# Performance work log

Measured on AMD Instinct MI355X. Metric: run time of the kernel, lower is better.

## Reference

```python
import jax, jax.numpy as jnp
import numpy as np

B, K, F, INCH, OUTCH, R = 16, 8, 512, 512, 512, 8


def setup_inputs() -> dict:
    key = jax.random.key(0)
    ks = jax.random.split(key, 10)
    inp = {
        "x": jax.random.normal(ks[0], (B, K, F, INCH), jnp.float32),
        "u": jax.random.normal(ks[1], (B, K, OUTCH, R), jnp.float32),
        "v": jax.random.normal(ks[2], (B, K, INCH, R), jnp.float32),
        "b": jax.random.normal(ks[3], (B, 1, 1, OUTCH), jnp.float32) * 0.02,
        # learned parameters (torch nn.Linear layout: W [out, in])
        "W_pass": jax.random.normal(ks[4], (INCH // 2, INCH), jnp.float32) * 0.02,
        "b_pass": jax.random.normal(ks[5], (INCH // 2,), jnp.float32) * 0.02,
        "W_ave": jax.random.normal(ks[6], (INCH // 2, INCH), jnp.float32) * 0.02,
        "b_ave": jax.random.normal(ks[7], (INCH // 2,), jnp.float32) * 0.02,
        "W_out": jax.random.normal(ks[8], (OUTCH, INCH), jnp.float32) * 0.02,
        "b_out": jax.random.normal(ks[9], (OUTCH,), jnp.float32) * 0.02,
    }
    return inp


def reference(x, u, v, b, W_pass, b_pass, W_ave, b_ave, W_out, b_out):
    # x: [B,K,F,inch]
    k = x.shape[1]
    # 'ave' branch: linear -> mean over K -> broadcast back to K
    y = jnp.einsum('bkfi,hi->bkfh', x, W_ave) + b_ave        # [B,K,F,inch//2]
    y = jnp.broadcast_to(jnp.mean(y, axis=1, keepdims=True), y.shape)
    # 'pass' branch
    xp = jnp.einsum('bkfi,hi->bkfh', x, W_pass) + b_pass      # [B,K,F,inch//2]
    h = jnp.concatenate([xp, y], axis=-1)                     # [B,K,F,inch]
    h = jax.nn.gelu(h, approximate=False)                     # dropout is identity in eval
    # LoRA term: mean(v * h) over inch, then mean(u * z) over R
    inch = h.shape[-1]
    r = v.shape[-1]
    z = jnp.einsum('bkfi,bkir->bkfr', h, v) / inch            # [B,K,F,R]
    lora = jnp.einsum('bkfr,bkor->bkfo', z, u) / r            # [B,K,F,outch]
    out = jnp.einsum('bkfi,oi->bkfo', h, W_out) + b_out + lora + b
    out = jax.nn.gelu(out, approximate=False)
    return out
```

## Files before the change

kernel.cpp:

```cpp
#include <hip/hip_runtime.h>
#include <stdint.h>


typedef __attribute__((ext_vector_type(8))) __bf16 bf16x8;
typedef __attribute__((ext_vector_type(4))) float f32x4;
typedef __attribute__((ext_vector_type(8))) unsigned short ushort8;
typedef __attribute__((ext_vector_type(4))) unsigned short ushort4_t;
typedef __attribute__((ext_vector_type(4))) float float4_t;

#define MFMA16(a, b, c) __builtin_amdgcn_mfma_f32_16x16x32_bf16((a), (b), (c), 0, 0, 0)
#define GLL16(g, l)                                                                   \
    __builtin_amdgcn_global_load_lds((const __attribute__((address_space(1))) void*)(g), \
                                     (__attribute__((address_space(3))) void*)(l), 16, 0, 0)

__device__ inline unsigned short f2bf(float f) {
    union { float fv; unsigned u; } un; un.fv = f;
    unsigned u = un.u;
    u += 0x7FFFu + ((u >> 16) & 1u);
    return (unsigned short)(u >> 16);
}

__device__ inline float geluf(float x) {
    float x2 = x * x;
    float inner = x + 0.044715f * x * x2;
    float e = __expf(-1.5957691216057308f * inner);
    return x * __builtin_amdgcn_rcpf(1.0f + e);
}

__device__ inline bf16x8 lds8(const unsigned short* p) {
    return __builtin_bit_cast(bf16x8, *(const ushort8*)p);
}

__device__ inline void stage_w(const unsigned short* __restrict__ src, long rowbase,
                               long stride, int k0, unsigned short* buf, int l) {
#pragma unroll
    for (int it = 0; it < 4; ++it) {
        const int s = it * 64 + l;
        const int r = s >> 2;
        const int j = (s & 3) ^ (r & 3);
        GLL16(src + (rowbase + r) * stride + k0 + j * 8, &buf[it * 512]);
    }
}

__device__ inline bf16x8 ldw(const unsigned short* buf, int rbase, int l) {
    const int r = rbase + (l & 15);
    const int j = l >> 4;
    return lds8(&buf[r * 32 + (((j ^ r) & 3) << 3)]);
}

__global__ void cvt_all(const float* __restrict__ a, const float* __restrict__ b,
                        const float* __restrict__ c, unsigned short* __restrict__ oa,
                        unsigned short* __restrict__ ob, unsigned short* __restrict__ oc) {
    int bid = blockIdx.x;
    const float* s; unsigned short* d; int off;
    if (bid < 128) { s = a; d = oa; off = bid; }
    else if (bid < 256) { s = b; d = ob; off = bid - 128; }
    else { s = c; d = oc; off = bid - 256; }
    int i = off * 256 + threadIdx.x;
    float4_t v = *(const float4_t*)(s + (size_t)i * 4);
    ushort4_t r;
    r[0] = f2bf(v[0]); r[1] = f2bf(v[1]); r[2] = f2bf(v[2]); r[3] = f2bf(v[3]);
    *(ushort4_t*)(d + (size_t)i * 4) = r;
}

__global__ void mean_cvt(const float* __restrict__ x,
                         unsigned short* __restrict__ xb,
                         unsigned short* __restrict__ xm) {
    int gid = blockIdx.x * 256 + threadIdx.x;
    int c  = gid & 63;
    int bf = gid >> 6;
    int b  = bf >> 9;
    int f  = bf & 511;
    float s0 = 0.f, s1 = 0.f, s2 = 0.f, s3 = 0.f, s4 = 0.f, s5 = 0.f, s6 = 0.f, s7 = 0.f;
#pragma unroll
    for (int k = 0; k < 8; ++k) {
        long row = (long)(b * 8 + k) * 512 + f;
        float4_t lo = *(const float4_t*)(x + row * 512 + c * 8);
        float4_t hi = *(const float4_t*)(x + row * 512 + c * 8 + 4);
        s0 += lo[0]; s1 += lo[1]; s2 += lo[2]; s3 += lo[3];
        s4 += hi[0]; s5 += hi[1]; s6 += hi[2]; s7 += hi[3];
        ushort8 t;
        t[0] = f2bf(lo[0]); t[1] = f2bf(lo[1]); t[2] = f2bf(lo[2]); t[3] = f2bf(lo[3]);
        t[4] = f2bf(hi[0]); t[5] = f2bf(hi[1]); t[6] = f2bf(hi[2]); t[7] = f2bf(hi[3]);
        *(ushort8*)(xb + row * 512 + c * 8) = t;
    }
    ushort8 m;
    m[0] = f2bf(s0 * 0.125f); m[1] = f2bf(s1 * 0.125f);
    m[2] = f2bf(s2 * 0.125f); m[3] = f2bf(s3 * 0.125f);
    m[4] = f2bf(s4 * 0.125f); m[5] = f2bf(s5 * 0.125f);
    m[6] = f2bf(s6 * 0.125f); m[7] = f2bf(s7 * 0.125f);
    *(ushort8*)(xm + (long)bf * 512 + c * 8) = m;
}

__launch_bounds__(256)
__global__ void gemm_gelu(const unsigned short* __restrict__ A,
                          const unsigned short* __restrict__ W,
                          const float* __restrict__ bias,
                          unsigned short* __restrict__ O,
                          int chunk) {
    __shared__ __align__(16) unsigned short S[32768];
    const int tid = threadIdx.x;
    const int w = tid >> 6, l = tid & 63;
    const int wr = w >> 1, wc = w & 1;
    const int work = ((blockIdx.x & 7) * chunk) + (blockIdx.x >> 3);
    const int nt = work & 1;
    const int mt = work >> 1;
    const long row0 = (long)mt * 128 + wr * 64;
    const long col0 = (long)nt * 128 + wc * 64;

    unsigned short* aw[2] = { &S[w * 4096],        &S[16384 + w * 4096] };
    unsigned short* bw[2] = { &S[w * 4096 + 2048], &S[16384 + w * 4096 + 2048] };

    f32x4 acc[4][4];
    const f32x4 z4 = {0.f, 0.f, 0.f, 0.f};
#pragma unroll
    for (int i = 0; i < 4; ++i)
#pragma unroll
        for (int j = 0; j < 4; ++j) acc[i][j] = z4;

    stage_w(A, row0, 512, 0, aw[0], l);
    stage_w(W, col0, 512, 0, bw[0], l);

#pragma unroll
    for (int t = 0; t < 16; ++t) {
        if (t < 15) {
            stage_w(A, row0, 512, (t + 1) * 32, aw[(t + 1) & 1], l);
            stage_w(W, col0, 512, (t + 1) * 32, bw[(t + 1) & 1], l);
            asm volatile("s_waitcnt vmcnt(8)" ::: "memory");
        } else {
            asm volatile("s_waitcnt vmcnt(0)" ::: "memory");
        }
        const unsigned short* ab = aw[t & 1];
        const unsigned short* bb = bw[t & 1];
        bf16x8 af[4], bfr[4];
#pragma unroll
        for (int mi = 0; mi < 4; ++mi) af[mi] = ldw(ab, mi * 16, l);
#pragma unroll
        for (int nj = 0; nj < 4; ++nj) bfr[nj] = ldw(bb, nj * 16, l);
        __builtin_amdgcn_s_setprio(1);
#pragma unroll
        for (int mi = 0; mi < 4; ++mi)
#pragma unroll
            for (int nj = 0; nj < 4; ++nj)
                acc[mi][nj] = MFMA16(af[mi], bfr[nj], acc[mi][nj]);
        __builtin_amdgcn_s_setprio(0);
    }

    __syncthreads();
#pragma unroll
    for (int mi = 0; mi < 4; ++mi) {
        const int R0 = wr * 64 + mi * 16 + (l >> 4) * 4;
#pragma unroll
        for (int nj = 0; nj < 4; ++nj) {
            const int C = wc * 64 + nj * 16 + (l & 15);
            const float bv = bias[((col0 & ~63L) - wc * 64) + C];
#pragma unroll
            for (int q = 0; q < 4; ++q)
                S[(R0 + q) * 136 + C] = f2bf(geluf(acc[mi][nj][q] + bv));
        }
    }
    __syncthreads();
    const long rowt = (long)mt * 128;
    const long colt = (long)nt * 128;
#pragma unroll
    for (int s = 0; s < 8; ++s) {
        const int flat = s * 2048 + tid * 8;
        const int row = flat >> 7;
        const int col = flat & 127;
        ushort8 vv = *(const ushort8*)&S[row * 136 + col];
        *(ushort8*)(O + (rowt + row) * 256 + colt + col) = vv;
    }
}

__launch_bounds__(256)
__global__ void zcalc_s(const unsigned short* __restrict__ Hp,
                        const unsigned short* __restrict__ Gy,
                        const float* __restrict__ v,
                        unsigned short* __restrict__ zb) {
    __shared__ __align__(16) unsigned short Vt[16 * 536];
    const int tid = threadIdx.x;
    const int w = tid >> 6, l = tid & 63;
    const int mt = blockIdx.x;
    const long row0 = (long)mt * 128;
    const int gb = (mt >> 5) * 512 + (mt & 3) * 128;
    {
        ushort8 zz = {0, 0, 0, 0, 0, 0, 0, 0};
        for (int i = tid; i < (16 * 536) / 8; i += 256) *(ushort8*)&Vt[i * 8] = zz;
        __syncthreads();
        const float* vp = v + (long)(mt >> 2) * 4096;
#pragma unroll
        for (int p = 0; p < 4; ++p) {
            float4_t vv = *(const float4_t*)(vp + tid * 16 + p * 4);
#pragma unroll
            for (int j = 0; j < 4; ++j) {
                int flat = tid * 16 + p * 4 + j;
                Vt[(flat & 7) * 536 + (flat >> 3)] = f2bf(vv[j] * (1.0f / 512.0f));
            }
        }
        __syncthreads();
    }
    const unsigned short* ph[2];
    const unsigned short* pg[2];
#pragma unroll
    for (int q = 0; q < 2; ++q) {
        const int r = (w * 2 + q) * 16 + (l & 15);
        ph[q] = Hp + (row0 + r) * 256 + (l >> 4) * 8;
        pg[q] = Gy + (size_t)(gb + r) * 256 + (l >> 4) * 8;
    }
    f32x4 zacc[2];
    const f32x4 z4 = {0.f, 0.f, 0.f, 0.f};
    zacc[0] = z4; zacc[1] = z4;
#pragma unroll
    for (int ks = 0; ks < 8; ++ks) {
        bf16x8 bv = lds8(&Vt[(l & 15) * 536 + ks * 32 + (l >> 4) * 8]);
#pragma unroll
        for (int q = 0; q < 2; ++q)
            zacc[q] = MFMA16(lds8(ph[q] + ks * 32), bv, zacc[q]);
    }
#pragma unroll
    for (int ks = 0; ks < 8; ++ks) {
        bf16x8 bv = lds8(&Vt[(l & 15) * 536 + 256 + ks * 32 + (l >> 4) * 8]);
#pragma unroll
        for (int q = 0; q < 2; ++q)
            zacc[q] = MFMA16(lds8(pg[q] + ks * 32), bv, zacc[q]);
    }
    if ((l & 15) < 8) {
#pragma unroll
        for (int q = 0; q < 2; ++q) {
            const int fr = w * 2 + q;
#pragma unroll
            for (int reg = 0; reg < 4; ++reg) {
                long r = row0 + fr * 16 + (l >> 4) * 4 + reg;
                zb[r * 8 + (l & 15)] = f2bf(zacc[q][reg]);
            }
        }
    }
}

__launch_bounds__(256)
__global__ void gemm_out(const unsigned short* __restrict__ Hp,
                         const unsigned short* __restrict__ Gy,
                         const unsigned short* __restrict__ Wo,
                         const float* __restrict__ bo,
                         const float* __restrict__ bb,
                         const float* __restrict__ u,
                         const unsigned short* __restrict__ zb,
                         float* __restrict__ Out) {
    __shared__ __align__(16) char SM[67584];
    unsigned short* S = (unsigned short*)SM;
    float* Sf = (float*)SM;
    const int tid = threadIdx.x;
    const int w = tid >> 6, l = tid & 63;
    const int wr = w >> 1, wc = w & 1;
    const int work = ((blockIdx.x & 7) * 256) + (blockIdx.x >> 3);
    const int nt = work & 3;
    const int mt = work >> 2;
    const long row0 = (long)mt * 128;
    const long arow = row0 + wr * 64;
    const long grow = (long)((mt >> 5) * 512 + (mt & 3) * 128) + wr * 64;
    const long col0 = (long)nt * 128 + wc * 64;
    const int bk = mt >> 2;
    const int bi = bk >> 3;

    unsigned short* aw[2] = { &S[w * 4096],        &S[16384 + w * 4096] };
    unsigned short* bw[2] = { &S[w * 4096 + 2048], &S[16384 + w * 4096 + 2048] };

    f32x4 acc[4][4];
    const f32x4 z4 = {0.f, 0.f, 0.f, 0.f};
#pragma unroll
    for (int i = 0; i < 4; ++i)
#pragma unroll
        for (int j = 0; j < 4; ++j) acc[i][j] = z4;

    stage_w(Hp, arow, 256, 0, aw[0], l);
    stage_w(Wo, col0, 512, 0, bw[0], l);

#pragma unroll
    for (int t = 0; t < 16; ++t) {
        if (t < 15) {
            const int tt = t + 1;
            if (tt < 8) stage_w(Hp, arow, 256, tt * 32, aw[tt & 1], l);
            else        stage_w(Gy, grow, 256, (tt - 8) * 32, aw[tt & 1], l);
            stage_w(Wo, col0, 512, tt * 32, bw[tt & 1], l);
            asm volatile("s_waitcnt vmcnt(8)" ::: "memory");
        } else {
            asm volatile("s_waitcnt vmcnt(0)" ::: "memory");
        }
        const unsigned short* ab = aw[t & 1];
        const unsigned short* bbuf = bw[t & 1];
        bf16x8 af[4], bfr[4];
#pragma unroll
        for (int mi = 0; mi < 4; ++mi) af[mi] = ldw(ab, mi * 16, l);
#pragma unroll
        for (int nj = 0; nj < 4; ++nj) bfr[nj] = ldw(bbuf, nj * 16, l);
        __builtin_amdgcn_s_setprio(1);
#pragma unroll
        for (int mi = 0; mi < 4; ++mi)
#pragma unroll
            for (int nj = 0; nj < 4; ++nj)
                acc[mi][nj] = MFMA16(af[mi], bfr[nj], acc[mi][nj]);
        __builtin_amdgcn_s_setprio(0);
    }

    __syncthreads();
    {
        ushort8 zz = {0, 0, 0, 0, 0, 0, 0, 0};
        const int row = tid >> 1;
        if ((tid & 1) == 0) {
            *(ushort8*)&S[row * 32]     = *(const ushort8*)&zb[(row0 + row) * 8];
            *(ushort8*)&S[row * 32 + 8] = zz;
        } else {
            *(ushort8*)&S[row * 32 + 16] = zz;
            *(ushort8*)&S[row * 32 + 24] = zz;
        }
    }
    __syncthreads();

    const float* up = u + (long)bk * 4096;
#pragma unroll
    for (int nj = 0; nj < 4; ++nj) {
        const long og = col0 + nj * 16 + (l & 15);
        ushort8 ubits = {0, 0, 0, 0, 0, 0, 0, 0};
        if ((l >> 4) == 0) {
            float4_t u0 = *(const float4_t*)(up + og * 8);
            float4_t u1 = *(const float4_t*)(up + og * 8 + 4);
            ubits[0] = f2bf(u0[0] * 0.125f); ubits[1] = f2bf(u0[1] * 0.125f);
            ubits[2] = f2bf(u0[2] * 0.125f); ubits[3] = f2bf(u0[3] * 0.125f);
            ubits[4] = f2bf(u1[0] * 0.125f); ubits[5] = f2bf(u1[1] * 0.125f);
            ubits[6] = f2bf(u1[2] * 0.125f); ubits[7] = f2bf(u1[3] * 0.125f);
        }
        bf16x8 ub = __builtin_bit_cast(bf16x8, ubits);
#pragma unroll
        for (int mi = 0; mi < 4; ++mi) {
            bf16x8 az = lds8(&S[(wr * 64 + mi * 16 + (l & 15)) * 32 + (l >> 4) * 8]);
            acc[mi][nj] = MFMA16(az, ub, acc[mi][nj]);
        }
    }

    __syncthreads();
#pragma unroll
    for (int nj = 0; nj < 4; ++nj) {
        const long og = col0 + nj * 16 + (l & 15);
        const float badd = bo[og] + bb[bi * 512 + og];
        const int C = wc * 64 + nj * 16 + (l & 15);
#pragma unroll
        for (int mi = 0; mi < 4; ++mi) {
            const int R0 = wr * 64 + mi * 16 + (l >> 4) * 4;
#pragma unroll
            for (int q = 0; q < 4; ++q)
                Sf[(R0 + q) * 132 + C] = geluf(acc[mi][nj][q] + badd);
        }
    }
    __syncthreads();
    const long colt = (long)nt * 128;
#pragma unroll
    for (int s = 0; s < 16; ++s) {
        const int flat = s * 1024 + tid * 4;
        const int row = flat >> 7;
        const int col = flat & 127;
        float4_t vv = *(const float4_t*)&Sf[row * 132 + col];
        __builtin_nontemporal_store(vv, (float4_t*)(Out + (row0 + row) * 512 + colt + col));
    }
}

extern "C" void kernel_launch(void* const* d_in, const int* in_sizes, int n_in,
                              void* d_out, int out_size, void* d_ws, size_t ws_size,
                              hipStream_t stream) {
    const float* x  = (const float*)d_in[0];
    const float* u  = (const float*)d_in[1];
    const float* v  = (const float*)d_in[2];
    const float* bb = (const float*)d_in[3];
    const float* Wp = (const float*)d_in[4];
    const float* bp = (const float*)d_in[5];
    const float* Wa = (const float*)d_in[6];
    const float* ba = (const float*)d_in[7];
    const float* Wo = (const float*)d_in[8];
    const float* bo = (const float*)d_in[9];
    float* out = (float*)d_out;

    char* ws = (char*)d_ws;
    unsigned short* xb  = (unsigned short*)(ws + 0);
    unsigned short* zb  = (unsigned short*)(ws + 0);
    unsigned short* xm  = (unsigned short*)(ws + 67108864);
    unsigned short* gy  = (unsigned short*)(ws + 75497472);
    unsigned short* hp  = (unsigned short*)(ws + 79691776);
    unsigned short* Wpb = (unsigned short*)(ws + 113246208);
    unsigned short* Wab = (unsigned short*)(ws + 113508352);
    unsigned short* Wob = (unsigned short*)(ws + 113770496);

    cvt_all<<<512, 256, 0, stream>>>(Wp, Wa, Wo, Wpb, Wab, Wob);
    mean_cvt<<<2048, 256, 0, stream>>>(x, xb, xm);
    gemm_gelu<<<128, 256, 0, stream>>>(xm, Wab, ba, gy, 16);
    gemm_gelu<<<1024, 256, 0, stream>>>(xb, Wpb, bp, hp, 128);
    zcalc_s<<<512, 256, 0, stream>>>(hp, gy, v, zb);
    gemm_out<<<2048, 256, 0, stream>>>(hp, gy, Wob, bo, bb, u, zb, out);
}
```

Before: 169.0 us.

## Load GEMM operands directly from global into registers with 3-stage prefetch

```diff
diff --git a/kernel.cpp b/kernel.cpp
--- a/kernel.cpp
+++ b/kernel.cpp
@@ -9,9 +9,6 @@
 typedef __attribute__((ext_vector_type(4))) float float4_t;
 
 #define MFMA16(a, b, c) __builtin_amdgcn_mfma_f32_16x16x32_bf16((a), (b), (c), 0, 0, 0)
-#define GLL16(g, l)                                                                   \
-    __builtin_amdgcn_global_load_lds((const __attribute__((address_space(1))) void*)(g), \
-                                     (__attribute__((address_space(3))) void*)(l), 16, 0, 0)
 
 __device__ inline unsigned short f2bf(float f) {
     union { float fv; unsigned u; } un; un.fv = f;
@@ -29,23 +26,6 @@
 
 __device__ inline bf16x8 lds8(const unsigned short* p) {
     return __builtin_bit_cast(bf16x8, *(const ushort8*)p);
-}
-
-__device__ inline void stage_w(const unsigned short* __restrict__ src, long rowbase,
-                               long stride, int k0, unsigned short* buf, int l) {
-#pragma unroll
-    for (int it = 0; it < 4; ++it) {
-        const int s = it * 64 + l;
-        const int r = s >> 2;
-        const int j = (s & 3) ^ (r & 3);
-        GLL16(src + (rowbase + r) * stride + k0 + j * 8, &buf[it * 512]);
-    }
-}
-
-__device__ inline bf16x8 ldw(const unsigned short* buf, int rbase, int l) {
-    const int r = rbase + (l & 15);
-    const int j = l >> 4;
-    return lds8(&buf[r * 32 + (((j ^ r) & 3) << 3)]);
 }
 
 __global__ void cvt_all(const float* __restrict__ a, const float* __restrict__ b,
@@ -92,13 +72,13 @@
     *(ushort8*)(xm + (long)bf * 512 + c * 8) = m;
 }
 
-__launch_bounds__(256)
+__launch_bounds__(256, 2)
 __global__ void gemm_gelu(const unsigned short* __restrict__ A,
                           const unsigned short* __restrict__ W,
                           const float* __restrict__ bias,
                           unsigned short* __restrict__ O,
                           int chunk) {
-    __shared__ __align__(16) unsigned short S[32768];
+    __shared__ __align__(16) unsigned short S[17408];
     const int tid = threadIdx.x;
     const int w = tid >> 6, l = tid & 63;
     const int wr = w >> 1, wc = w & 1;
@@ -108,8 +88,8 @@
     const long row0 = (long)mt * 128 + wr * 64;
     const long col0 = (long)nt * 128 + wc * 64;
 
-    unsigned short* aw[2] = { &S[w * 4096],        &S[16384 + w * 4096] };
-    unsigned short* bw[2] = { &S[w * 4096 + 2048], &S[16384 + w * 4096 + 2048] };
+    const unsigned short* abase = A + (row0 + (l & 15)) * 512 + (l >> 4) * 8;
+    const unsigned short* wbase = W + (col0 + (l & 15)) * 512 + (l >> 4) * 8;
 
     f32x4 acc[4][4];
     const f32x4 z4 = {0.f, 0.f, 0.f, 0.f};
@@ -118,42 +98,47 @@
 #pragma unroll
         for (int j = 0; j < 4; ++j) acc[i][j] = z4;
 
-    stage_w(A, row0, 512, 0, aw[0], l);
-    stage_w(W, col0, 512, 0, bw[0], l);
+    ushort8 ap[3][4], bp[3][4];
+
+#define LDAB_G(st, t)                                                          \
+    {                                                                          \
+        _Pragma("unroll") for (int mi = 0; mi < 4; ++mi)                       \
+            ap[st][mi] = *(const ushort8*)(abase + mi * 8192 + (t) * 32);      \
+        _Pragma("unroll") for (int nj = 0; nj < 4; ++nj)                       \
+            bp[st][nj] = *(const ushort8*)(wbase + nj * 8192 + (t) * 32);      \
+    }
+
+    LDAB_G(0, 0)
+    LDAB_G(1, 1)
+    LDAB_G(2, 2)
 
 #pragma unroll
     for (int t = 0; t < 16; ++t) {
-        if (t < 15) {
-            stage_w(A, row0, 512, (t + 1) * 32, aw[(t + 1) & 1], l);
-            stage_w(W, col0, 512, (t + 1) * 32, bw[(t + 1) & 1], l);
-            asm volatile("s_waitcnt vmcnt(8)" ::: "memory");
-        } else {
-            asm volatile("s_waitcnt vmcnt(0)" ::: "memory");
-        }
-        const unsigned short* ab = aw[t & 1];
-        const unsigned short* bb = bw[t & 1];
-        bf16x8 af[4], bfr[4];
-#pragma unroll
-        for (int mi = 0; mi < 4; ++mi) af[mi] = ldw(ab, mi * 16, l);
-#pragma unroll
-        for (int nj = 0; nj < 4; ++nj) bfr[nj] = ldw(bb, nj * 16, l);
+        const int cs = t % 3;
+        bf16x8 a[4], b[4];
+#pragma unroll
+        for (int mi = 0; mi < 4; ++mi) a[mi] = __builtin_bit_cast(bf16x8, ap[cs][mi]);
+#pragma unroll
+        for (int nj = 0; nj < 4; ++nj) b[nj] = __builtin_bit_cast(bf16x8, bp[cs][nj]);
+        if (t + 3 < 16) LDAB_G(cs, t + 3)
         __builtin_amdgcn_s_setprio(1);
 #pragma unroll
         for (int mi = 0; mi < 4; ++mi)
 #pragma unroll
             for (int nj = 0; nj < 4; ++nj)
-                acc[mi][nj] = MFMA16(af[mi], bfr[nj], acc[mi][nj]);
+                acc[mi][nj] = MFMA16(a[mi], b[nj], acc[mi][nj]);
         __builtin_amdgcn_s_setprio(0);
     }
-
-    __syncthreads();
+#undef LDAB_G
+
+    const int colblk = nt * 128;
 #pragma unroll
     for (int mi = 0; mi < 4; ++mi) {
         const int R0 = wr * 64 + mi * 16 + (l >> 4) * 4;
 #pragma unroll
         for (int nj = 0; nj < 4; ++nj) {
             const int C = wc * 64 + nj * 16 + (l & 15);
-            const float bv = bias[((col0 & ~63L) - wc * 64) + C];
+            const float bv = bias[colblk + C];
 #pragma unroll
             for (int q = 0; q < 4; ++q)
                 S[(R0 + q) * 136 + C] = f2bf(geluf(acc[mi][nj][q] + bv));
@@ -161,14 +146,13 @@
     }
     __syncthreads();
     const long rowt = (long)mt * 128;
-    const long colt = (long)nt * 128;
 #pragma unroll
     for (int s = 0; s < 8; ++s) {
         const int flat = s * 2048 + tid * 8;
         const int row = flat >> 7;
         const int col = flat & 127;
         ushort8 vv = *(const ushort8*)&S[row * 136 + col];
-        *(ushort8*)(O + (rowt + row) * 256 + colt + col) = vv;
+        *(ushort8*)(O + (rowt + row) * 256 + colblk + col) = vv;
     }
 }
 
@@ -237,7 +221,7 @@
     }
 }
 
-__launch_bounds__(256)
+__launch_bounds__(256, 2)
 __global__ void gemm_out(const unsigned short* __restrict__ Hp,
                          const unsigned short* __restrict__ Gy,
                          const unsigned short* __restrict__ Wo,
@@ -262,8 +246,9 @@
     const int bk = mt >> 2;
     const int bi = bk >> 3;
 
-    unsigned short* aw[2] = { &S[w * 4096],        &S[16384 + w * 4096] };
-    unsigned short* bw[2] = { &S[w * 4096 + 2048], &S[16384 + w * 4096 + 2048] };
+    const unsigned short* hbase = Hp + (arow + (l & 15)) * 256 + (l >> 4) * 8;
+    const unsigned short* gbase = Gy + (grow + (l & 15)) * 256 + (l >> 4) * 8;
+    const unsigned short* wbase = Wo + (col0 + (l & 15)) * 512 + (l >> 4) * 8;
 
     f32x4 acc[4][4];
     const f32x4 z4 = {0.f, 0.f, 0.f, 0.f};
@@ -272,37 +257,41 @@
 #pragma unroll
         for (int j = 0; j < 4; ++j) acc[i][j] = z4;
 
-    stage_w(Hp, arow, 256, 0, aw[0], l);
-    stage_w(Wo, col0, 512, 0, bw[0], l);
+    ushort8 ap[3][4], bp[3][4];
+
+#define LDAB_O(st, t)                                                            \
+    {                                                                            \
+        const unsigned short* ab_ =                                              \
+            ((t) < 8) ? (hbase + (t) * 32) : (gbase + ((t) - 8) * 32);           \
+        _Pragma("unroll") for (int mi = 0; mi < 4; ++mi)                         \
+            ap[st][mi] = *(const ushort8*)(ab_ + mi * 4096);                     \
+        _Pragma("unroll") for (int nj = 0; nj < 4; ++nj)                         \
+            bp[st][nj] = *(const ushort8*)(wbase + nj * 8192 + (t) * 32);        \
+    }
+
+    LDAB_O(0, 0)
+    LDAB_O(1, 1)
+    LDAB_O(2, 2)
 
 #pragma unroll
     for (int t = 0; t < 16; ++t) {
-        if (t < 15) {
-            const int tt = t + 1;
-            if (tt < 8) stage_w(Hp, arow, 256, tt * 32, aw[tt & 1], l);
-            else        stage_w(Gy, grow, 256, (tt - 8) * 32, aw[tt & 1], l);
-            stage_w(Wo, col0, 512, tt * 32, bw[tt & 1], l);
-            asm volatile("s_waitcnt vmcnt(8)" ::: "memory");
-        } else {
-            asm volatile("s_waitcnt vmcnt(0)" ::: "memory");
-        }
-        const unsigned short* ab = aw[t & 1];
-        const unsigned short* bbuf = bw[t & 1];
-        bf16x8 af[4], bfr[4];
-#pragma unroll
-        for (int mi = 0; mi < 4; ++mi) af[mi] = ldw(ab, mi * 16, l);
-#pragma unroll
-        for (int nj = 0; nj < 4; ++nj) bfr[nj] = ldw(bbuf, nj * 16, l);
+        const int cs = t % 3;
+        bf16x8 a[4], b[4];
+#pragma unroll
+        for (int mi = 0; mi < 4; ++mi) a[mi] = __builtin_bit_cast(bf16x8, ap[cs][mi]);
+#pragma unroll
+        for (int nj = 0; nj < 4; ++nj) b[nj] = __builtin_bit_cast(bf16x8, bp[cs][nj]);
+        if (t + 3 < 16) LDAB_O(cs, t + 3)
         __builtin_amdgcn_s_setprio(1);
 #pragma unroll
         for (int mi = 0; mi < 4; ++mi)
 #pragma unroll
             for (int nj = 0; nj < 4; ++nj)
-                acc[mi][nj] = MFMA16(af[mi], bfr[nj], acc[mi][nj]);
+                acc[mi][nj] = MFMA16(a[mi], b[nj], acc[mi][nj]);
         __builtin_amdgcn_s_setprio(0);
     }
-
-    __syncthreads();
+#undef LDAB_O
+
     {
         ushort8 zz = {0, 0, 0, 0, 0, 0, 0, 0};
         const int row = tid >> 1;
```

Result: slower. 257.8 us (+52.6%).

## Precompute K-invariant averaged-branch output projection once per batch

Applied to the files above, without the earlier changes.

```diff
diff --git a/kernel.cpp b/kernel.cpp
--- a/kernel.cpp
+++ b/kernel.cpp
@@ -147,13 +147,14 @@
     }
 
     __syncthreads();
+    const int colblk = nt * 128;
 #pragma unroll
     for (int mi = 0; mi < 4; ++mi) {
         const int R0 = wr * 64 + mi * 16 + (l >> 4) * 4;
 #pragma unroll
         for (int nj = 0; nj < 4; ++nj) {
             const int C = wc * 64 + nj * 16 + (l & 15);
-            const float bv = bias[((col0 & ~63L) - wc * 64) + C];
+            const float bv = bias[colblk + C];
 #pragma unroll
             for (int q = 0; q < 4; ++q)
                 S[(R0 + q) * 136 + C] = f2bf(geluf(acc[mi][nj][q] + bv));
@@ -161,14 +162,13 @@
     }
     __syncthreads();
     const long rowt = (long)mt * 128;
-    const long colt = (long)nt * 128;
 #pragma unroll
     for (int s = 0; s < 8; ++s) {
         const int flat = s * 2048 + tid * 8;
         const int row = flat >> 7;
         const int col = flat & 127;
         ushort8 vv = *(const ushort8*)&S[row * 136 + col];
-        *(ushort8*)(O + (rowt + row) * 256 + colt + col) = vv;
+        *(ushort8*)(O + (rowt + row) * 256 + colblk + col) = vv;
     }
 }
 
@@ -238,13 +238,76 @@
 }
 
 __launch_bounds__(256)
+__global__ void g2calc(const unsigned short* __restrict__ Gy,
+                       const unsigned short* __restrict__ Wo,
+                       const float* __restrict__ bo,
+                       float* __restrict__ G2) {
+    __shared__ __align__(16) unsigned short S[32768];
+    const int tid = threadIdx.x;
+    const int w = tid >> 6, l = tid & 63;
+    const int wr = w >> 1, wc = w & 1;
+    const int mt = blockIdx.x >> 2;
+    const int nt = blockIdx.x & 3;
+    const long row0 = (long)mt * 128 + wr * 64;
+    const long col0 = (long)nt * 128 + wc * 64;
+
+    unsigned short* aw[2] = { &S[w * 4096],        &S[16384 + w * 4096] };
+    unsigned short* bw[2] = { &S[w * 4096 + 2048], &S[16384 + w * 4096 + 2048] };
+
+    f32x4 acc[4][4];
+    const f32x4 z4 = {0.f, 0.f, 0.f, 0.f};
+#pragma unroll
+    for (int i = 0; i < 4; ++i)
+#pragma unroll
+        for (int j = 0; j < 4; ++j) acc[i][j] = z4;
+
+    stage_w(Gy, row0, 256, 0, aw[0], l);
+    stage_w(Wo, col0, 512, 256, bw[0], l);
+
+#pragma unroll
+    for (int t = 0; t < 8; ++t) {
+        if (t < 7) {
+            stage_w(Gy, row0, 256, (t + 1) * 32, aw[(t + 1) & 1], l);
+            stage_w(Wo, col0, 512, 256 + (t + 1) * 32, bw[(t + 1) & 1], l);
+            asm volatile("s_waitcnt vmcnt(8)" ::: "memory");
+        } else {
+            asm volatile("s_waitcnt vmcnt(0)" ::: "memory");
+        }
+        const unsigned short* ab = aw[t & 1];
+        const unsigned short* bbuf = bw[t & 1];
+        bf16x8 af[4], bfr[4];
+#pragma unroll
+        for (int mi = 0; mi < 4; ++mi) af[mi] = ldw(ab, mi * 16, l);
+#pragma unroll
+        for (int nj = 0; nj < 4; ++nj) bfr[nj] = ldw(bbuf, nj * 16, l);
+#pragma unroll
+        for (int mi = 0; mi < 4; ++mi)
+#pragma unroll
+            for (int nj = 0; nj < 4; ++nj)
+                acc[mi][nj] = MFMA16(af[mi], bfr[nj], acc[mi][nj]);
+    }
+
+#pragma unroll
+    for (int mi = 0; mi < 4; ++mi) {
+        const long rb = row0 + mi * 16 + (l >> 4) * 4;
+#pragma unroll
+        for (int nj = 0; nj < 4; ++nj) {
+            const long cg = col0 + nj * 16 + (l & 15);
+            const float bv = bo[cg];
+#pragma unroll
+            for (int q = 0; q < 4; ++q)
+                G2[(rb + q) * 512 + cg] = acc[mi][nj][q] + bv;
+        }
+    }
+}
+
+__launch_bounds__(256)
 __global__ void gemm_out(const unsigned short* __restrict__ Hp,
-                         const unsigned short* __restrict__ Gy,
                          const unsigned short* __restrict__ Wo,
-                         const float* __restrict__ bo,
                          const float* __restrict__ bb,
                          const float* __restrict__ u,
                          const unsigned short* __restrict__ zb,
+                         const float* __restrict__ G2,
                          float* __restrict__ Out) {
     __shared__ __align__(16) char SM[67584];
     unsigned short* S = (unsigned short*)SM;
@@ -257,8 +320,8 @@
     const int mt = work >> 2;
     const long row0 = (long)mt * 128;
     const long arow = row0 + wr * 64;
-    const long grow = (long)((mt >> 5) * 512 + (mt & 3) * 128) + wr * 64;
     const long col0 = (long)nt * 128 + wc * 64;
+    const int g2b = (mt >> 5) * 512 + (mt & 3) * 128;
     const int bk = mt >> 2;
     const int bi = bk >> 3;
 
@@ -276,12 +339,10 @@
     stage_w(Wo, col0, 512, 0, bw[0], l);
 
 #pragma unroll
-    for (int t = 0; t < 16; ++t) {
-        if (t < 15) {
-            const int tt = t + 1;
-            if (tt < 8) stage_w(Hp, arow, 256, tt * 32, aw[tt & 1], l);
-            else        stage_w(Gy, grow, 256, (tt - 8) * 32, aw[tt & 1], l);
-            stage_w(Wo, col0, 512, tt * 32, bw[tt & 1], l);
+    for (int t = 0; t < 8; ++t) {
+        if (t < 7) {
+            stage_w(Hp, arow, 256, (t + 1) * 32, aw[(t + 1) & 1], l);
+            stage_w(Wo, col0, 512, (t + 1) * 32, bw[(t + 1) & 1], l);
             asm volatile("s_waitcnt vmcnt(8)" ::: "memory");
         } else {
             asm volatile("s_waitcnt vmcnt(0)" ::: "memory");
@@ -341,14 +402,14 @@
 #pragma unroll
     for (int nj = 0; nj < 4; ++nj) {
         const long og = col0 + nj * 16 + (l & 15);
-        const float badd = bo[og] + bb[bi * 512 + og];
+        const float badd = bb[bi * 512 + og];
         const int C = wc * 64 + nj * 16 + (l & 15);
 #pragma unroll
         for (int mi = 0; mi < 4; ++mi) {
             const int R0 = wr * 64 + mi * 16 + (l >> 4) * 4;
 #pragma unroll
             for (int q = 0; q < 4; ++q)
-                Sf[(R0 + q) * 132 + C] = geluf(acc[mi][nj][q] + badd);
+                Sf[(R0 + q) * 132 + C] = acc[mi][nj][q] + badd;
         }
     }
     __syncthreads();
@@ -359,7 +420,11 @@
         const int row = flat >> 7;
         const int col = flat & 127;
         float4_t vv = *(const float4_t*)&Sf[row * 132 + col];
-        __builtin_nontemporal_store(vv, (float4_t*)(Out + (row0 + row) * 512 + colt + col));
+        float4_t g4 = *(const float4_t*)(G2 + (size_t)(g2b + row) * 512 + colt + col);
+        float4_t o4;
+        o4[0] = geluf(vv[0] + g4[0]); o4[1] = geluf(vv[1] + g4[1]);
+        o4[2] = geluf(vv[2] + g4[2]); o4[3] = geluf(vv[3] + g4[3]);
+        __builtin_nontemporal_store(o4, (float4_t*)(Out + (row0 + row) * 512 + colt + col));
     }
 }
 
@@ -381,6 +446,7 @@
     char* ws = (char*)d_ws;
     unsigned short* xb  = (unsigned short*)(ws + 0);
     unsigned short* zb  = (unsigned short*)(ws + 0);
+    float*          G2  = (float*)(ws + 2097152);
     unsigned short* xm  = (unsigned short*)(ws + 67108864);
     unsigned short* gy  = (unsigned short*)(ws + 75497472);
     unsigned short* hp  = (unsigned short*)(ws + 79691776);
@@ -392,6 +458,7 @@
     mean_cvt<<<2048, 256, 0, stream>>>(x, xb, xm);
     gemm_gelu<<<128, 256, 0, stream>>>(xm, Wab, ba, gy, 16);
     gemm_gelu<<<1024, 256, 0, stream>>>(xb, Wpb, bp, hp, 128);
+    g2calc<<<256, 256, 0, stream>>>(gy, Wob, bo, G2);
     zcalc_s<<<512, 256, 0, stream>>>(hp, gy, v, zb);
-    gemm_out<<<2048, 256, 0, stream>>>(hp, gy, Wob, bo, bb, u, zb, out);
-}
+    gemm_out<<<2048, 256, 0, stream>>>(hp, Wob, bb, u, zb, G2, out);
+}
```

Result: no change. 168.7 us (-0.2%).
